# Performance work log

Hardware: AMD Instinct MI355X
Metric: run time of the kernel (lower is better)

The kernel has to match this reference:

```python
import jax, jax.numpy as jnp
import numpy as np

B, S, D, H = 2, 2048, 1024, 16
HD = D // H  # 64


def setup_inputs() -> dict:
    key = jax.random.key(0)
    ks = jax.random.split(key, 10)
    sc = 1.0 / np.sqrt(D)
    return {
        "decoder_hs": jax.random.normal(ks[0], (B, S, D), jnp.float32),
        "encoder_hs": jax.random.normal(ks[1], (B, S, D), jnp.float32),
        "Wq": jax.random.normal(ks[2], (D, D), jnp.float32) * sc,
        "bq": jax.random.normal(ks[3], (D,), jnp.float32) * 0.02,
        "Wk": jax.random.normal(ks[4], (D, D), jnp.float32) * sc,
        "bk": jax.random.normal(ks[5], (D,), jnp.float32) * 0.02,
        "Wv": jax.random.normal(ks[6], (D, D), jnp.float32) * sc,
        "bv": jax.random.normal(ks[7], (D,), jnp.float32) * 0.02,
        "Wp": jax.random.normal(ks[8], (D, D), jnp.float32) * sc,
        "bp": jax.random.normal(ks[9], (D,), jnp.float32) * 0.02,
    }


def reference(decoder_hs, encoder_hs, Wq, bq, Wk, bk, Wv, bv, Wp, bp):
    b, s, d = decoder_hs.shape
    # torch nn.Linear: y = x @ W.T + b, W is [out, in]
    q = decoder_hs @ Wq.T + bq
    k = encoder_hs @ Wk.T + bk
    v = encoder_hs @ Wv.T + bv
    # head split: [b, s, d] -> [b, h, s, hd]
    q = q.reshape(b, s, H, HD).transpose(0, 2, 1, 3)
    k = k.reshape(b, s, H, HD).transpose(0, 2, 1, 3)
    v = v.reshape(b, s, H, HD).transpose(0, 2, 1, 3)
    scale = 1.0 / np.sqrt(HD).astype(np.float32)
    att = jnp.einsum('bhqd,bhkd->bhqk', q, k) * scale
    att = jax.nn.softmax(att, axis=-1)
    y = jnp.einsum('bhqk,bhkd->bhqd', att, v)
    y = y.transpose(0, 2, 1, 3).reshape(b, s, d)
    return y @ Wp.T + bp
```

## Files before the change

### kernel.cpp

```cpp
#include <hip/hip_runtime.h>
#include <hip/hip_bf16.h>
#include <cstdint>
#include <cstddef>

#define BB 2
#define SS 2048
#define DD 1024
#define HH 16
#define HD 64

typedef __attribute__((ext_vector_type(8))) short bf16x8;
typedef __attribute__((ext_vector_type(4))) short bf16x4;
typedef __attribute__((ext_vector_type(4))) float f32x4;

#define MFMA16(va, vb, c) __builtin_amdgcn_mfma_f32_16x16x16bf16_1k(va, vb, c, 0, 0, 0)

#define GLL(g, l) __builtin_amdgcn_global_load_lds( \
    (const __attribute__((address_space(1))) void*)(g), \
    (__attribute__((address_space(3))) void*)(l), 16, 0, 0)

__device__ __forceinline__ short f2bf_fast(float f) {
    uint32_t u = __float_as_uint(f);
    u += 0x7FFF + ((u >> 16) & 1);
    return (short)(u >> 16);
}
__device__ __forceinline__ uint32_t pack_bf2(float a, float b) {
    uint32_t ua = __float_as_uint(a), ub = __float_as_uint(b);
    ua += 0x7FFF + ((ua >> 16) & 1);
    ub += 0x7FFF + ((ub >> 16) & 1);
    return (ua >> 16) | (ub & 0xFFFF0000u);
}
__device__ __forceinline__ bf16x8 cvt8(const float* __restrict__ p) {
    float4 a = *(const float4*)p;
    float4 b = *(const float4*)(p + 4);
    union { uint32_t d[4]; bf16x8 v; } r;
    r.d[0] = pack_bf2(a.x, a.y);
    r.d[1] = pack_bf2(a.z, a.w);
    r.d[2] = pack_bf2(b.x, b.y);
    r.d[3] = pack_bf2(b.z, b.w);
    return r.v;
}

__global__ __launch_bounds__(256) void cvt6_kernel(
    const float* __restrict__ s0, const float* __restrict__ s1,
    const float* __restrict__ s2, const float* __restrict__ s3,
    const float* __restrict__ s4, const float* __restrict__ s5,
    short* __restrict__ d0, short* __restrict__ d1, short* __restrict__ d2,
    short* __restrict__ d3, short* __restrict__ d4, short* __restrict__ d5)
{
    const int z = blockIdx.z;
    const float* s = (z == 0) ? s0 : (z == 1) ? s1 : (z == 2) ? s2
                   : (z == 3) ? s3 : (z == 4) ? s4 : s5;
    short* d = (z == 0) ? d0 : (z == 1) ? d1 : (z == 2) ? d2
             : (z == 3) ? d3 : (z == 4) ? d4 : d5;
    const int n8 = (z < 2) ? (BB * SS * DD / 8) : (DD * DD / 8);
    const int id = blockIdx.x * 256 + threadIdx.x;
    if (id >= n8) return;
    bf16x8 r = cvt8(s + (size_t)id * 8);
    *(uint4*)(d + (size_t)id * 8) = *(uint4*)&r;
}

template<int BF>
__global__ __launch_bounds__(256, 3) void qkv_gemm_kernel(
    const void* __restrict__ dec, const void* __restrict__ enc,
    const void* __restrict__ Wq, const void* __restrict__ Wk,
    const void* __restrict__ Wv,
    const float* __restrict__ bq, const float* __restrict__ bk,
    const float* __restrict__ bv,
    short* __restrict__ Qo, short* __restrict__ Ko, short* __restrict__ Vo)
{
    __shared__ short As[128 * 32];
    __shared__ short Bs[128 * 32];

    const int z = blockIdx.z;
    const void* Xv = (z == 0) ? dec : enc;
    const void* Wp_ = (z == 0) ? Wq : (z == 1) ? Wk : Wv;
    const float* bias = (z == 0) ? bq : (z == 1) ? bk : bv;
    short* Yo = (z == 0) ? Qo : (z == 1) ? Ko : Vo;

    const int t = threadIdx.x;
    const int lane = t & 63, wv = t >> 6;
    const int lr = lane & 15, quad = lane >> 4;
    const int wm = wv >> 1, wn = wv & 1;
    const int m0 = blockIdx.y * 128;
    const int n0 = blockIdx.x * 128;
    const int K = DD;

    f32x4 acc[4][4];
    #pragma unroll
    for (int i = 0; i < 4; i++)
        #pragma unroll
        for (int j = 0; j < 4; j++) acc[i][j] = (f32x4){0.f, 0.f, 0.f, 0.f};

    for (int kb = 0; kb < K; kb += 32) {
        __syncthreads();
        if (BF) {
            const short* Xb = (const short*)Xv;
            const short* Wb = (const short*)Wp_;
            #pragma unroll
            for (int c = 0; c < 2; c++) {
                int r0 = wv * 32 + c * 16;
                int r = r0 + (lane >> 2), ch = (lane & 3) * 8;
                GLL(Xb + (size_t)(m0 + r) * K + kb + ch, &As[r0 * 32]);
                GLL(Wb + (size_t)(n0 + r) * K + kb + ch, &Bs[r0 * 32]);
            }
        } else {
            const float* Xf = (const float*)Xv;
            const float* Wf = (const float*)Wp_;
            #pragma unroll
            for (int c = 0; c < 2; c++) {
                int id = t + c * 256;
                int r = id >> 2, c8 = (id & 3) * 8;
                *(bf16x8*)&As[r * 32 + c8] = cvt8(Xf + (size_t)(m0 + r) * K + kb + c8);
                *(bf16x8*)&Bs[r * 32 + c8] = cvt8(Wf + (size_t)(n0 + r) * K + kb + c8);
            }
        }
        __syncthreads();

        bf16x8 af[4], bfr[4];
        #pragma unroll
        for (int mi = 0; mi < 4; mi++)
            af[mi] = *(const bf16x8*)&As[(wm * 64 + mi * 16 + lr) * 32 + quad * 8];
        #pragma unroll
        for (int ni = 0; ni < 4; ni++)
            bfr[ni] = *(const bf16x8*)&Bs[(wn * 64 + ni * 16 + lr) * 32 + quad * 8];
        #pragma unroll
        for (int mi = 0; mi < 4; mi++)
            #pragma unroll
            for (int ni = 0; ni < 4; ni++)
                acc[mi][ni] = __builtin_amdgcn_mfma_f32_16x16x32_bf16(
                    af[mi], bfr[ni], acc[mi][ni], 0, 0, 0);
    }

    if (z < 2) {
        #pragma unroll
        for (int ni = 0; ni < 4; ni++) {
            int col = n0 + wn * 64 + ni * 16 + lr;
            int h = col >> 6, hd = col & 63;
            float bvv = bias[col];
            #pragma unroll
            for (int mi = 0; mi < 4; mi++) {
                #pragma unroll
                for (int r2 = 0; r2 < 4; r2++) {
                    int row = m0 + wm * 64 + mi * 16 + quad * 4 + r2;
                    int b = row >> 11, s = row & 2047;
                    float v = acc[mi][ni][r2] + bvv;
                    size_t off = ((size_t)(b * HH + h) * SS + s) * HD + hd;
                    Yo[off] = f2bf_fast(v);
                }
            }
        }
    } else {
        #pragma unroll
        for (int ni = 0; ni < 4; ni++) {
            int col = n0 + wn * 64 + ni * 16 + lr;
            int h = col >> 6, hd = col & 63;
            float bvv = bias[col];
            #pragma unroll
            for (int mi = 0; mi < 4; mi++) {
                int s0 = m0 + wm * 64 + mi * 16 + quad * 4;
                int b = s0 >> 11, s = s0 & 2047;
                union { uint32_t d[2]; } u;
                u.d[0] = pack_bf2(acc[mi][ni][0] + bvv, acc[mi][ni][1] + bvv);
                u.d[1] = pack_bf2(acc[mi][ni][2] + bvv, acc[mi][ni][3] + bvv);
                size_t off = ((size_t)(b * HH + h) * HD + hd) * SS + s;
                *(uint2*)(Yo + off) = *(uint2*)&u;
            }
        }
    }
}

template<int WBF>
__global__ __launch_bounds__(256, 2) void proj_gemm_kernel(
    const short* __restrict__ X,
    const void* __restrict__ W, const float* __restrict__ bias,
    float* __restrict__ Y)
{
    __shared__ short As[64 * 32];
    __shared__ short Bs[128 * 32];

    const int t = threadIdx.x;
    const int lane = t & 63, wv = t >> 6;
    const int lr = lane & 15, quad = lane >> 4;
    const int wm = wv >> 1, wn = wv & 1;
    const int m0 = blockIdx.y * 64;
    const int n0 = blockIdx.x * 128;
    const int K = DD, N = DD;

    f32x4 acc[2][4];
    #pragma unroll
    for (int i = 0; i < 2; i++)
        #pragma unroll
        for (int j = 0; j < 4; j++) acc[i][j] = (f32x4){0.f, 0.f, 0.f, 0.f};

    for (int kb = 0; kb < K; kb += 32) {
        __syncthreads();
        {
            int r0 = wv * 16;
            int r = r0 + (lane >> 2), ch = (lane & 3) * 8;
            GLL(X + (size_t)(m0 + r) * K + kb + ch, &As[r0 * 32]);
        }
        if (WBF) {
            const short* Wb = (const short*)W;
            #pragma unroll
            for (int c = 0; c < 2; c++) {
                int r0 = wv * 32 + c * 16;
                int r = r0 + (lane >> 2), ch = (lane & 3) * 8;
                GLL(Wb + (size_t)(n0 + r) * K + kb + ch, &Bs[r0 * 32]);
            }
        } else {
            const float* Wf = (const float*)W;
            #pragma unroll
            for (int c = 0; c < 2; c++) {
                int id = t + c * 256;
                int r = id >> 2, c8 = (id & 3) * 8;
                *(bf16x8*)&Bs[r * 32 + c8] = cvt8(Wf + (size_t)(n0 + r) * K + kb + c8);
            }
        }
        __syncthreads();

        bf16x8 af[2], bfr[4];
        #pragma unroll
        for (int mi = 0; mi < 2; mi++)
            af[mi] = *(const bf16x8*)&As[(wm * 32 + mi * 16 + lr) * 32 + quad * 8];
        #pragma unroll
        for (int ni = 0; ni < 4; ni++)
            bfr[ni] = *(const bf16x8*)&Bs[(wn * 64 + ni * 16 + lr) * 32 + quad * 8];
        #pragma unroll
        for (int mi = 0; mi < 2; mi++)
            #pragma unroll
            for (int ni = 0; ni < 4; ni++)
                acc[mi][ni] = __builtin_amdgcn_mfma_f32_16x16x32_bf16(
                    af[mi], bfr[ni], acc[mi][ni], 0, 0, 0);
    }

    #pragma unroll
    for (int ni = 0; ni < 4; ni++) {
        int col = n0 + wn * 64 + ni * 16 + lr;
        float bvv = bias[col];
        #pragma unroll
        for (int mi = 0; mi < 2; mi++) {
            #pragma unroll
            for (int r2 = 0; r2 < 4; r2++) {
                int row = m0 + wm * 32 + mi * 16 + quad * 4 + r2;
                Y[(size_t)row * N + col] = acc[mi][ni][r2] + bvv;
            }
        }
    }
}

__global__ __launch_bounds__(256, 2) void attn_kernel(
    const short* __restrict__ Q,
    const short* __restrict__ Kgl,
    const short* __restrict__ Vt_g,
    short* __restrict__ Y)
{
    __shared__ short Ks[2][128][64];
    __shared__ short Vt[2][64][128];

    const int t = threadIdx.x;
    const int lane = t & 63, w = t >> 6;
    const int lr = lane & 15, quad = lane >> 4;
    const int e = lr & 7;

    const int bid = blockIdx.x;
    const int slot = bid >> 3;
    const int bh = ((slot >> 4) << 3) + (bid & 7);
    const int qt = slot & 15;
    const int b = bh >> 4, h = bh & 15;

    const float C = 0.125f * 1.44269504088896f;

    const short* QpA = Q + ((size_t)bh * SS + qt * 128 + w * 32 + lr) * HD;
    const short* QpB = QpA + 16 * HD;
    bf16x8 qfA0 = *(const bf16x8*)(QpA + quad * 8);
    bf16x8 qfA1 = *(const bf16x8*)(QpA + 32 + quad * 8);
    bf16x8 qfB0 = *(const bf16x8*)(QpB + quad * 8);
    bf16x8 qfB1 = *(const bf16x8*)(QpB + 32 + quad * 8);

    f32x4 oA[4], oB[4];
    #pragma unroll
    for (int i = 0; i < 4; i++) {
        oA[i] = (f32x4){0.f, 0.f, 0.f, 0.f};
        oB[i] = (f32x4){0.f, 0.f, 0.f, 0.f};
    }
    float lsumA = 0.f, lsumB = 0.f;

    const short* Kb = Kgl + (size_t)bh * SS * HD;
    const short* Vb = Vt_g + (size_t)bh * HD * SS;

    auto stage = [&](int kt1, int nb) {
        #pragma unroll
        for (int c = 0; c < 4; c++) {
            int r0 = w * 32 + c * 8;
            int r  = r0 + (lane >> 3);
            int sc = ((lane & 7) ^ (r & 7)) * 8;
            GLL(Kb + (size_t)(kt1 * 128 + r) * 64 + sc, &Ks[nb][r0][0]);
        }
        #pragma unroll
        for (int c = 0; c < 4; c++) {
            int h0 = w * 16 + c * 4;
            int hd = h0 + (lane >> 4);
            int s16 = (lane & 15) ^ (hd & 7);
            GLL(Vb + (size_t)hd * SS + kt1 * 128 + s16 * 8, &Vt[nb][h0][0]);
        }
    };

    stage(0, 0);
    __syncthreads();

    int cur = 0;
    for (int kt = 0; kt < SS / 128; kt++) {
        if (kt + 1 < SS / 128) stage(kt + 1, cur ^ 1);

        f32x4 scA[8], scB[8];
        #pragma unroll
        for (int nt = 0; nt < 8; nt++) {
            const short* krow = &Ks[cur][nt * 16 + lr][0];
            bf16x8 kf0 = *(const bf16x8*)&krow[(quad ^ e) * 8];
            bf16x8 kf1 = *(const bf16x8*)&krow[((quad + 4) ^ e) * 8];
            scA[nt] = __builtin_amdgcn_mfma_f32_16x16x32_bf16(
                kf0, qfA0, (f32x4){0.f, 0.f, 0.f, 0.f}, 0, 0, 0);
            scA[nt] = __builtin_amdgcn_mfma_f32_16x16x32_bf16(kf1, qfA1, scA[nt], 0, 0, 0);
            scB[nt] = __builtin_amdgcn_mfma_f32_16x16x32_bf16(
                kf0, qfB0, (f32x4){0.f, 0.f, 0.f, 0.f}, 0, 0, 0);
            scB[nt] = __builtin_amdgcn_mfma_f32_16x16x32_bf16(kf1, qfB1, scB[nt], 0, 0, 0);
        }

        bf16x4 pbA[8], pbB[8];
        #pragma unroll
        for (int nt = 0; nt < 8; nt++) {
            float a0 = __builtin_amdgcn_exp2f(scA[nt][0] * C);
            float a1 = __builtin_amdgcn_exp2f(scA[nt][1] * C);
            float a2 = __builtin_amdgcn_exp2f(scA[nt][2] * C);
            float a3 = __builtin_amdgcn_exp2f(scA[nt][3] * C);
            lsumA += (a0 + a1) + (a2 + a3);
            union { uint32_t d[2]; bf16x4 v; } ua;
            ua.d[0] = pack_bf2(a0, a1);
            ua.d[1] = pack_bf2(a2, a3);
            pbA[nt] = ua.v;
            float b0 = __builtin_amdgcn_exp2f(scB[nt][0] * C);
            float b1 = __builtin_amdgcn_exp2f(scB[nt][1] * C);
            float b2 = __builtin_amdgcn_exp2f(scB[nt][2] * C);
            float b3 = __builtin_amdgcn_exp2f(scB[nt][3] * C);
            lsumB += (b0 + b1) + (b2 + b3);
            union { uint32_t d[2]; bf16x4 v; } ub;
            ub.d[0] = pack_bf2(b0, b1);
            ub.d[1] = pack_bf2(b2, b3);
            pbB[nt] = ub.v;
        }

        #pragma unroll
        for (int dt = 0; dt < 4; dt++) {
            const short* vrow = &Vt[cur][dt * 16 + lr][0];
            #pragma unroll
            for (int nt = 0; nt < 8; nt++) {
                int ch = (nt * 2 + (quad >> 1)) ^ e;
                bf16x4 va = *(const bf16x4*)&vrow[ch * 8 + (quad & 1) * 4];
                oA[dt] = MFMA16(va, pbA[nt], oA[dt]);
                oB[dt] = MFMA16(va, pbB[nt], oB[dt]);
            }
        }

        __syncthreads();
        cur ^= 1;
    }

    lsumA += __shfl_xor(lsumA, 16, 64);
    lsumA += __shfl_xor(lsumA, 32, 64);
    lsumB += __shfl_xor(lsumB, 16, 64);
    lsumB += __shfl_xor(lsumB, 32, 64);
    float invA = 1.0f / lsumA, invB = 1.0f / lsumB;

    const int srowA = qt * 128 + w * 32 + lr;
    short* YpA = Y + ((size_t)b * SS + srowA) * DD + h * 64 + quad * 4;
    short* YpB = YpA + 16 * DD;
    #pragma unroll
    for (int dt = 0; dt < 4; dt++) {
        union { uint32_t d[2]; } ua;
        ua.d[0] = pack_bf2(oA[dt][0] * invA, oA[dt][1] * invA);
        ua.d[1] = pack_bf2(oA[dt][2] * invA, oA[dt][3] * invA);
        *(uint2*)(YpA + dt * 16) = *(uint2*)&ua;
        union { uint32_t d[2]; } ub;
        ub.d[0] = pack_bf2(oB[dt][0] * invB, oB[dt][1] * invB);
        ub.d[1] = pack_bf2(oB[dt][2] * invB, oB[dt][3] * invB);
        *(uint2*)(YpB + dt * 16) = *(uint2*)&ub;
    }
}

extern "C" void kernel_launch(void* const* d_in, const int* in_sizes, int n_in,
                              void* d_out, int out_size, void* d_ws, size_t ws_size,
                              hipStream_t stream) {
    const float* dec = (const float*)d_in[0];
    const float* enc = (const float*)d_in[1];
    const float* Wq  = (const float*)d_in[2];
    const float* bq  = (const float*)d_in[3];
    const float* Wk  = (const float*)d_in[4];
    const float* bk  = (const float*)d_in[5];
    const float* Wv  = (const float*)d_in[6];
    const float* bv  = (const float*)d_in[7];
    const float* Wp  = (const float*)d_in[8];
    const float* bp  = (const float*)d_in[9];

    const size_t per = (size_t)BB * HH * SS * HD;
    const size_t wsz = (size_t)DD * DD;
    short* ws = (short*)d_ws;
    short* Qb  = ws;
    short* Kb  = ws + per;
    short* Vtb = ws + 2 * per;
    short* Yb  = ws + 3 * per;

    dim3 qkv_grid(DD / 128, (BB * SS) / 128, 3);
    dim3 proj_grid(DD / 128, (BB * SS) / 64);
    const int attn_blocks = BB * HH * (SS / 128);

    const size_t need = (6 * per + 4 * wsz) * sizeof(short);
    if (ws_size >= need) {
        short* decb = ws + 4 * per;
        short* encb = ws + 5 * per;
        short* Wqb  = ws + 6 * per;
        short* Wkb  = Wqb + wsz;
        short* Wvb  = Wqb + 2 * wsz;
        short* Wpb  = Wqb + 3 * wsz;
        cvt6_kernel<<<dim3((BB * SS * DD / 8 + 255) / 256, 1, 6), 256, 0, stream>>>(
            dec, enc, Wq, Wk, Wv, Wp, decb, encb, Wqb, Wkb, Wvb, Wpb);
        qkv_gemm_kernel<1><<<qkv_grid, 256, 0, stream>>>(
            decb, encb, Wqb, Wkb, Wvb, bq, bk, bv, Qb, Kb, Vtb);
        attn_kernel<<<attn_blocks, 256, 0, stream>>>(Qb, Kb, Vtb, Yb);
        proj_gemm_kernel<1><<<proj_grid, 256, 0, stream>>>(Yb, Wpb, bp, (float*)d_out);
    } else {
        qkv_gemm_kernel<0><<<qkv_grid, 256, 0, stream>>>(
            dec, enc, Wq, Wk, Wv, bq, bk, bv, Qb, Kb, Vtb);
        attn_kernel<<<attn_blocks, 256, 0, stream>>>(Qb, Kb, Vtb, Yb);
        proj_gemm_kernel<0><<<proj_grid, 256, 0, stream>>>(Yb, Wp, bp, (float*)d_out);
    }
}
```

Baseline: 212.3 us.

## Fold softmax scale into Q projection, use hardware bf16 pack and MFMA priority

The softmax scale (1/sqrt(hd)·log2e) moves into the Q GEMM epilogue, so the attention inner loop no longer multiplies every score before exp2. The software round-to-bf16 packing of probabilities is replaced by the v_cvt_pk_bf16_f32 instruction. Row sums are kept in vector accumulators to shorten the dependency chain. s_setprio raises wave priority around the MFMA blocks. Rounding Q after scaling slightly changes numerics, and the inline asm ties the code to targets that have this instruction.

```diff
diff --git a/kernel.cpp b/kernel.cpp
--- a/kernel.cpp
+++ b/kernel.cpp
@@ -29,6 +29,11 @@
     ua += 0x7FFF + ((ua >> 16) & 1);
     ub += 0x7FFF + ((ub >> 16) & 1);
     return (ua >> 16) | (ub & 0xFFFF0000u);
+}
+__device__ __forceinline__ uint32_t cvtpk_bf2(float a, float b) {
+    uint32_t r;
+    asm("v_cvt_pk_bf16_f32 %0, %1, %2" : "=v"(r) : "v"(a), "v"(b));
+    return r;
 }
 __device__ __forceinline__ bf16x8 cvt8(const float* __restrict__ p) {
     float4 a = *(const float4*)p;
@@ -77,6 +82,7 @@
     const void* Wp_ = (z == 0) ? Wq : (z == 1) ? Wk : Wv;
     const float* bias = (z == 0) ? bq : (z == 1) ? bk : bv;
     short* Yo = (z == 0) ? Qo : (z == 1) ? Ko : Vo;
+    const float qs = (z == 0) ? (0.125f * 1.44269504088896f) : 1.0f;
 
     const int t = threadIdx.x;
     const int lane = t & 63, wv = t >> 6;
@@ -144,7 +150,7 @@
                 for (int r2 = 0; r2 < 4; r2++) {
                     int row = m0 + wm * 64 + mi * 16 + quad * 4 + r2;
                     int b = row >> 11, s = row & 2047;
-                    float v = acc[mi][ni][r2] + bvv;
+                    float v = (acc[mi][ni][r2] + bvv) * qs;
                     size_t off = ((size_t)(b * HH + h) * SS + s) * HD + hd;
                     Yo[off] = f2bf_fast(v);
                 }
@@ -269,8 +275,6 @@
     const int qt = slot & 15;
     const int b = bh >> 4, h = bh & 15;
 
-    const float C = 0.125f * 1.44269504088896f;
-
     const short* QpA = Q + ((size_t)bh * SS + qt * 128 + w * 32 + lr) * HD;
     const short* QpB = QpA + 16 * HD;
     bf16x8 qfA0 = *(const bf16x8*)(QpA + quad * 8);
@@ -284,7 +288,8 @@
         oA[i] = (f32x4){0.f, 0.f, 0.f, 0.f};
         oB[i] = (f32x4){0.f, 0.f, 0.f, 0.f};
     }
-    float lsumA = 0.f, lsumB = 0.f;
+    f32x4 vsumA = (f32x4){0.f, 0.f, 0.f, 0.f};
+    f32x4 vsumB = (f32x4){0.f, 0.f, 0.f, 0.f};
 
     const short* Kb = Kgl + (size_t)bh * SS * HD;
     const short* Vb = Vt_g + (size_t)bh * HD * SS;
@@ -314,6 +319,7 @@
         if (kt + 1 < SS / 128) stage(kt + 1, cur ^ 1);
 
         f32x4 scA[8], scB[8];
+        __builtin_amdgcn_s_setprio(1);
         #pragma unroll
         for (int nt = 0; nt < 8; nt++) {
             const short* krow = &Ks[cur][nt * 16 + lr][0];
@@ -326,30 +332,33 @@
                 kf0, qfB0, (f32x4){0.f, 0.f, 0.f, 0.f}, 0, 0, 0);
             scB[nt] = __builtin_amdgcn_mfma_f32_16x16x32_bf16(kf1, qfB1, scB[nt], 0, 0, 0);
         }
+        __builtin_amdgcn_s_setprio(0);
 
         bf16x4 pbA[8], pbB[8];
         #pragma unroll
         for (int nt = 0; nt < 8; nt++) {
-            float a0 = __builtin_amdgcn_exp2f(scA[nt][0] * C);
-            float a1 = __builtin_amdgcn_exp2f(scA[nt][1] * C);
-            float a2 = __builtin_amdgcn_exp2f(scA[nt][2] * C);
-            float a3 = __builtin_amdgcn_exp2f(scA[nt][3] * C);
-            lsumA += (a0 + a1) + (a2 + a3);
+            f32x4 ea, eb;
+            ea[0] = __builtin_amdgcn_exp2f(scA[nt][0]);
+            ea[1] = __builtin_amdgcn_exp2f(scA[nt][1]);
+            ea[2] = __builtin_amdgcn_exp2f(scA[nt][2]);
+            ea[3] = __builtin_amdgcn_exp2f(scA[nt][3]);
+            vsumA += ea;
             union { uint32_t d[2]; bf16x4 v; } ua;
-            ua.d[0] = pack_bf2(a0, a1);
-            ua.d[1] = pack_bf2(a2, a3);
+            ua.d[0] = cvtpk_bf2(ea[0], ea[1]);
+            ua.d[1] = cvtpk_bf2(ea[2], ea[3]);
             pbA[nt] = ua.v;
-            float b0 = __builtin_amdgcn_exp2f(scB[nt][0] * C);
-            float b1 = __builtin_amdgcn_exp2f(scB[nt][1] * C);
-            float b2 = __builtin_amdgcn_exp2f(scB[nt][2] * C);
-            float b3 = __builtin_amdgcn_exp2f(scB[nt][3] * C);
-            lsumB += (b0 + b1) + (b2 + b3);
+            eb[0] = __builtin_amdgcn_exp2f(scB[nt][0]);
+            eb[1] = __builtin_amdgcn_exp2f(scB[nt][1]);
+            eb[2] = __builtin_amdgcn_exp2f(scB[nt][2]);
+            eb[3] = __builtin_amdgcn_exp2f(scB[nt][3]);
+            vsumB += eb;
             union { uint32_t d[2]; bf16x4 v; } ub;
-            ub.d[0] = pack_bf2(b0, b1);
-            ub.d[1] = pack_bf2(b2, b3);
+            ub.d[0] = cvtpk_bf2(eb[0], eb[1]);
+            ub.d[1] = cvtpk_bf2(eb[2], eb[3]);
             pbB[nt] = ub.v;
         }
 
+        __builtin_amdgcn_s_setprio(1);
         #pragma unroll
         for (int dt = 0; dt < 4; dt++) {
             const short* vrow = &Vt[cur][dt * 16 + lr][0];
@@ -361,11 +370,14 @@
                 oB[dt] = MFMA16(va, pbB[nt], oB[dt]);
             }
         }
+        __builtin_amdgcn_s_setprio(0);
 
         __syncthreads();
         cur ^= 1;
     }
 
+    float lsumA = (vsumA[0] + vsumA[1]) + (vsumA[2] + vsumA[3]);
+    float lsumB = (vsumB[0] + vsumB[1]) + (vsumB[2] + vsumB[3]);
     lsumA += __shfl_xor(lsumA, 16, 64);
     lsumA += __shfl_xor(lsumA, 32, 64);
     lsumB += __shfl_xor(lsumB, 16, 64);
```

New measurement: 204.2 us. 3.8% less time.
